# Kernel optimization log

Measured on AMD Instinct MI355X. Metric: run time of the kernel, lower is better.

The kernel has to match this reference:

```python
import jax, jax.numpy as jnp
import numpy as np

N_NODES = 100
F_IN = 65536
C_OUT = 60
ACTION_DIM = 100
N_EDGES = 2000


def setup_inputs() -> dict:
    key = jax.random.key(0)
    ks = jax.random.split(key, 16)
    s = 0.02
    return {
        "substrate_features": jax.random.normal(ks[0], (1, N_NODES, F_IN), jnp.float32),
        "edge_index": jax.random.randint(ks[1], (2, N_EDGES), 0, N_NODES, dtype=jnp.int32),
        "v_cpu_demand_t": jax.random.uniform(ks[2], (1,), jnp.float32),
        "v_bw_demand_t": jax.random.uniform(ks[3], (1,), jnp.float32),
        "num_pending_v_nodes_t": jax.random.uniform(ks[4], (1,), jnp.float32),
        "actor_w": jax.random.normal(ks[5], (3, F_IN, C_OUT), jnp.float32) * s,
        "actor_b": jax.random.normal(ks[6], (C_OUT,), jnp.float32) * s,
        "critic_w": jax.random.normal(ks[7], (3, F_IN, C_OUT), jnp.float32) * s,
        "critic_b": jax.random.normal(ks[8], (C_OUT,), jnp.float32) * s,
        "actor_fc_w": jax.random.normal(ks[9], (N_NODES * C_OUT + 3, ACTION_DIM), jnp.float32) * s,
        "actor_fc_b": jax.random.normal(ks[10], (ACTION_DIM,), jnp.float32) * s,
        "critic_fc_w": jax.random.normal(ks[11], (N_NODES * C_OUT + 3, 1), jnp.float32) * s,
        "critic_fc_b": jax.random.normal(ks[12], (1,), jnp.float32) * s,
    }


def cheb_conv(x, edge_index, W, b):
    # ChebConv, K=3, sym normalization, lambda_max=2 (PyG defaults).
    # With lambda_max=2 the scaled Laplacian is L_hat = -D^{-1/2} A D^{-1/2}
    # (diagonal becomes 0 after the -1 self-loop shift).
    # x: [1, N, F]; edge_index: [2, E]; W: [3, F, C]; b: [C]
    src, dst = edge_index[0], edge_index[1]
    n = x.shape[1]
    deg = jax.ops.segment_sum(jnp.ones(src.shape[0], x.dtype), src, num_segments=n)
    dis = jnp.where(deg > 0, jax.lax.rsqrt(jnp.where(deg > 0, deg, 1.0)), 0.0)
    norm = -(dis[src] * dis[dst])  # [E], L_hat off-diagonal entries
    x2 = x[0]  # [N, F]

    def prop(z):  # z: [N, F] -> L_hat @ z via gather/scatter over edges
        return jax.ops.segment_sum(z[src] * norm[:, None], dst, num_segments=n)

    Tx0 = x2
    Tx1 = prop(Tx0)
    Tx2 = 2.0 * prop(Tx1) - Tx0
    out = Tx0 @ W[0] + Tx1 @ W[1] + Tx2 @ W[2] + b  # [N, C]
    return out[None]  # [1, N, C]


def reference(substrate_features, edge_index, v_cpu_demand_t, v_bw_demand_t,
              num_pending_v_nodes_t, actor_w, actor_b, critic_w, critic_b,
              actor_fc_w, actor_fc_b, critic_fc_w, critic_fc_b):
    emb_a = jnp.tanh(cheb_conv(substrate_features, edge_index, actor_w, actor_b))
    emb_a = emb_a.reshape(1, -1)  # [1, N*60]
    emb_c = jnp.tanh(cheb_conv(substrate_features, edge_index, critic_w, critic_b))
    emb_c = emb_c.reshape(1, -1)
    extras = [v_cpu_demand_t[None], v_bw_demand_t[None], num_pending_v_nodes_t[None]]  # each [1,1]
    state_a = jnp.concatenate([emb_a] + extras, axis=1)  # [1, 6003]
    state_c = jnp.concatenate([emb_c] + extras, axis=1)
    logits = state_a @ actor_fc_w + actor_fc_b  # [1, action_dim]
    values = state_c @ critic_fc_w + critic_fc_b  # [1, 1]
    return (logits, values)
```

## Files before the change

kernel.cpp:

```cpp
#include <hip/hip_runtime.h>
#include <stdint.h>

#define F_IN 65536
#define NN 100
#define CO 60
#define G_SPLIT 128
#define KC (F_IN/G_SPLIT)
#define BK 64
#define NIT (KC/BK)

typedef short v8s __attribute__((ext_vector_type(8)));
typedef float v4f __attribute__((ext_vector_type(4)));

__device__ __forceinline__ unsigned int f2bf(float x){
  unsigned int u = __float_as_uint(x);
  u += 0x7fffu + ((u>>16)&1u);
  return u>>16;
}
__device__ __forceinline__ v4f mfma16(v8s a, v8s b, v4f c){
  return __builtin_amdgcn_mfma_f32_16x16x32_bf16(a,b,c,0,0,0);
}
__device__ __forceinline__ void cp16(const void* g, void* l){
  __builtin_amdgcn_global_load_lds((const __attribute__((address_space(1))) void*)g,
                                   (__attribute__((address_space(3))) void*)l, 16, 0, 0);
}

__global__ __launch_bounds__(256)
void k_cvt(const float* __restrict__ x, unsigned short* __restrict__ xb){
  int i = blockIdx.x*256 + threadIdx.x;
  float4 v = ((const float4*)x)[i];
  uint2 w;
  w.x = f2bf(v.x) | (f2bf(v.y)<<16);
  w.y = f2bf(v.z) | (f2bf(v.w)<<16);
  ((uint2*)xb)[i] = w;
}

__global__ __launch_bounds__(256,2)
void k_gemm(const unsigned short* __restrict__ xb, const float* __restrict__ aw,
            const float* __restrict__ cw, float* __restrict__ dst, int partial){
  const int s = blockIdx.x, g = blockIdx.y;
  const int k0 = s*KC;
  const int tid = threadIdx.x, wave = tid>>6, lane = tid&63, quad = lane>>4, nl = lane&15;
  const int c0 = wave*16, ccl = min(c0+nl, CO-1);

  __shared__ __align__(16) unsigned short Ab[2][112*64];
  __shared__ __align__(16) float          Wb[2][BK*CO];

  const float* W = (g<3) ? (aw + (size_t)g*F_IN*CO) : (cw + (size_t)(g-3)*F_IN*CO);

  const int nA = (wave<2) ? 4 : 3;
  const int nW = (wave<3) ? 4 : 3;
  const unsigned short* ag[4];
  unsigned int aoff[4];
  #pragma unroll
  for(int ti=0; ti<4; ++ti){
    int t   = wave + 4*ti;
    int row = 8*t + (lane>>3);
    int rcl = min(row, NN-1);
    int lch = (lane&7) ^ (row&7);
    ag[ti]  = xb + (size_t)rcl*F_IN + k0 + lch*8;
    aoff[ti] = t*512 + lane*8;
  }
  const float* wg[4];
  unsigned int woff[4];
  #pragma unroll
  for(int ti=0; ti<4; ++ti){
    int t = wave + 4*ti;
    wg[ti]   = W + (size_t)k0*CO + t*256 + lane*4;
    woff[ti] = t*256 + lane*4;
  }

  v4f acc[7];
  #pragma unroll
  for(int i=0;i<7;++i){ v4f z={0.f,0.f,0.f,0.f}; acc[i]=z; }

  #pragma unroll
  for(int ti=0; ti<4; ++ti) if(ti<nA) cp16(ag[ti], &Ab[0][aoff[ti]]);
  #pragma unroll
  for(int ti=0; ti<4; ++ti) if(ti<nW) cp16(wg[ti], &Wb[0][woff[ti]]);

  for(int it=0; it<NIT; ++it){
    __syncthreads();
    const int b = it&1;
    if(it+1 < NIT){
      const int nb = (it+1)&1;
      #pragma unroll
      for(int ti=0; ti<4; ++ti) if(ti<nA) cp16(ag[ti] + (it+1)*BK, &Ab[nb][aoff[ti]]);
      #pragma unroll
      for(int ti=0; ti<4; ++ti) if(ti<nW) cp16(wg[ti] + (size_t)(it+1)*BK*CO, &Wb[nb][woff[ti]]);
    }
    v8s fB0, fB1;
    #pragma unroll
    for(int j=0;j<8;++j){
      fB0[j] = (short)f2bf(Wb[b][(   quad*8+j)*CO + ccl]);
      fB1[j] = (short)f2bf(Wb[b][(32+quad*8+j)*CO + ccl]);
    }
    #pragma unroll
    for(int mt=0; mt<7; ++mt){
      int r  = mt*16 + nl;
      int p0 = ((quad ^ (r&7))*8);
      v8s a0 = *(const v8s*)&Ab[b][r*64 + p0];
      v8s a1 = *(const v8s*)&Ab[b][r*64 + (p0^32)];
      acc[mt] = mfma16(a0, fB0, acc[mt]);
      acc[mt] = mfma16(a1, fB1, acc[mt]);
    }
  }

  const int c = c0 + nl;
  if(c < CO){
    if(partial){
      float* pd = dst + ((size_t)g*G_SPLIT + s)*(NN*CO);
      #pragma unroll
      for(int mt=0;mt<7;++mt){
        #pragma unroll
        for(int i=0;i<4;++i){
          int m = mt*16 + quad*4 + i;
          if(m < NN) pd[m*CO + c] = acc[mt][i];
        }
      }
    } else {
      float* pd = dst + (size_t)g*(NN*CO);
      #pragma unroll
      for(int mt=0;mt<7;++mt){
        #pragma unroll
        for(int i=0;i<4;++i){
          int m = mt*16 + quad*4 + i;
          if(m < NN) atomicAdd(pd + m*CO + c, acc[mt][i]);
        }
      }
    }
  }
}

__global__ void k_reduce(const float* __restrict__ P, float* __restrict__ Y){
  int o = blockIdx.x*256 + threadIdx.x;
  if(o >= 6*NN*CO) return;
  int gg = o/(NN*CO), r = o - gg*(NN*CO);
  const float* p = P + (size_t)gg*G_SPLIT*(NN*CO) + (size_t)blockIdx.y*32*(NN*CO) + r;
  float a0=0.f,a1=0.f,a2=0.f,a3=0.f;
  #pragma unroll 2
  for(int s4=0;s4<32;s4+=4){
    a0 += p[(s4  )*(NN*CO)];
    a1 += p[(s4+1)*(NN*CO)];
    a2 += p[(s4+2)*(NN*CO)];
    a3 += p[(s4+3)*(NN*CO)];
  }
  atomicAdd(&Y[o], (a0+a1)+(a2+a3));
}

__global__ void k_cheb(const float* __restrict__ Y, const int* __restrict__ ei,
                       const float* __restrict__ ab, const float* __restrict__ cb,
                       float* __restrict__ emb){
  const int net = blockIdx.x / CO;
  const int c   = blockIdx.x % CO;
  const int t   = threadIdx.x;
  __shared__ float L[NN][NN+1];
  __shared__ float dis[NN];
  __shared__ int   deg[NN];
  __shared__ float y0[NN], y1[NN], y2[NN], zu[NN];

  for(int i=t;i<NN*(NN+1);i+=128) ((float*)L)[i]=0.f;
  if(t<NN) deg[t]=0;
  __syncthreads();
  for(int e=t;e<2000;e+=128) atomicAdd(&deg[ei[e]],1);
  __syncthreads();
  if(t<NN) dis[t] = deg[t]>0 ? rsqrtf((float)deg[t]) : 0.f;
  __syncthreads();
  for(int e=t;e<2000;e+=128){
    int s = ei[e], d = ei[2000+e];
    atomicAdd(&L[d][s], -dis[s]*dis[d]);
  }
  if(t<NN){
    const float* yb = Y + (size_t)net*3*NN*CO + t*CO + c;
    y0[t]=yb[0]; y1[t]=yb[NN*CO]; y2[t]=yb[2*NN*CO];
  }
  __syncthreads();
  if(t<NN){
    float s=0.f;
    #pragma unroll 4
    for(int j=0;j<NN;++j) s += L[t][j]*y2[j];
    zu[t] = y1[t] + 2.f*s;
  }
  __syncthreads();
  if(t<NN){
    float s=0.f;
    #pragma unroll 4
    for(int j=0;j<NN;++j) s += L[t][j]*zu[j];
    float b = (net==0) ? ab[c] : cb[c];
    emb[net*NN*CO + t*CO + c] = tanhf(y0[t] - y2[t] + s + b);
  }
}

#define FCB 25
__global__ void k_fc(const float* __restrict__ emb, const float* __restrict__ afw,
                     const float* __restrict__ afb, const float* __restrict__ cfw,
                     const float* __restrict__ cfb, const float* __restrict__ s0,
                     const float* __restrict__ s1, const float* __restrict__ s2,
                     float* __restrict__ out){
  const int b = blockIdx.x;
  const int t = threadIdx.x;
  if(b < FCB){
    const int jj = t & 127, half = t >> 7;
    if(jj < 100){
      const int i0 = b*240 + half*120;
      const float* w = afw + (size_t)i0*100 + jj;
      const float* e = emb + i0;
      float p = 0.f;
      #pragma unroll 4
      for(int i=0;i<120;++i) p += e[i]*w[(size_t)i*100];
      atomicAdd(&out[jj], p);
    }
  } else {
    float p = 0.f;
    const float* e = emb + 6000;
    for(int i=t;i<6000;i+=256) p += e[i]*cfw[i];
    #pragma unroll
    for(int o=32;o>0;o>>=1) p += __shfl_down(p,o,64);
    __shared__ float red[4];
    if((t&63)==0) red[t>>6]=p;
    __syncthreads();
    if(t==0){
      float tot = red[0]+red[1]+red[2]+red[3];
      out[100] = tot + s0[0]*cfw[6000] + s1[0]*cfw[6001] + s2[0]*cfw[6002] + cfb[0];
    }
    if(t<100){
      atomicAdd(&out[t], afb[t] + s0[0]*afw[600000+t] + s1[0]*afw[600100+t] + s2[0]*afw[600200+t]);
    }
  }
}

extern "C" void kernel_launch(void* const* d_in, const int* in_sizes, int n_in,
                              void* d_out, int out_size, void* d_ws, size_t ws_size,
                              hipStream_t stream){
  const float* x   = (const float*)d_in[0];
  const int*   ei  = (const int*)d_in[1];
  const float* s0  = (const float*)d_in[2];
  const float* s1  = (const float*)d_in[3];
  const float* s2  = (const float*)d_in[4];
  const float* aw  = (const float*)d_in[5];
  const float* ab  = (const float*)d_in[6];
  const float* cw  = (const float*)d_in[7];
  const float* cb  = (const float*)d_in[8];
  const float* afw = (const float*)d_in[9];
  const float* afb = (const float*)d_in[10];
  const float* cfw = (const float*)d_in[11];
  const float* cfb = (const float*)d_in[12];
  float* out = (float*)d_out;

  unsigned short* xb = (unsigned short*)d_ws;
  float* Y   = (float*)((char*)d_ws + 13107200);
  float* emb = Y + 6*NN*CO;
  float* P   = emb + 2*NN*CO;
  const size_t need_full = 13107200u + (size_t)(6*NN*CO + 2*NN*CO)*4 + (size_t)6*G_SPLIT*NN*CO*4;
  const int partial = (ws_size >= need_full) ? 1 : 0;

  hipMemsetAsync(Y, 0, 6*NN*CO*sizeof(float), stream);
  hipMemsetAsync(out, 0, 101*sizeof(float), stream);

  k_cvt<<<6400, 256, 0, stream>>>(x, xb);
  k_gemm<<<dim3(G_SPLIT,6), 256, 0, stream>>>(xb, aw, cw, partial ? P : Y, partial);
  if(partial){
    k_reduce<<<dim3((6*NN*CO+255)/256, 4), 256, 0, stream>>>(P, Y);
  }
  k_cheb<<<120, 128, 0, stream>>>(Y, ei, ab, cb, emb);
  k_fc<<<FCB+1, 256, 0, stream>>>(emb, afw, afb, cfw, cfb, s0, s1, s2, out);
}
```

Baseline: 216.3 us.

## Triple-buffer the GEMM K loop with smaller K tiles and explicit vmcnt waits

Replaces the double-buffered LDS pipeline in the split-K GEMM with a three-stage ring buffer, halving the K tile to 32 and issuing loads two iterations ahead. It uses explicit s_waitcnt vmcnt and raw s_barrier with scheduling barriers instead of __syncthreads, so compute on one stage can overlap two in-flight global-to-LDS copies. Load work is redistributed so each wave issues exactly four 16-byte copies per stage, with some duplicated copies to keep the pattern uniform. The smaller tile and launch bound of 3 aim to raise occupancy and hide memory latency. The cost is more loop iterations and barriers per block.

```diff
diff --git a/kernel.cpp b/kernel.cpp
--- a/kernel.cpp
+++ b/kernel.cpp
@@ -6,8 +6,12 @@
 #define CO 60
 #define G_SPLIT 128
 #define KC (F_IN/G_SPLIT)
-#define BK 64
+#define BK 32
 #define NIT (KC/BK)
+#define NBUF 3
+#define ABYTES (112*BK*2)
+#define WBYTES (BK*CO*4)
+#define BUFB (ABYTES+WBYTES)
 
 typedef short v8s __attribute__((ext_vector_type(8)));
 typedef float v4f __attribute__((ext_vector_type(4)));
@@ -35,7 +39,7 @@
   ((uint2*)xb)[i] = w;
 }
 
-__global__ __launch_bounds__(256,2)
+__global__ __launch_bounds__(256,3)
 void k_gemm(const unsigned short* __restrict__ xb, const float* __restrict__ aw,
             const float* __restrict__ cw, float* __restrict__ dst, int partial){
   const int s = blockIdx.x, g = blockIdx.y;
@@ -43,68 +47,63 @@
   const int tid = threadIdx.x, wave = tid>>6, lane = tid&63, quad = lane>>4, nl = lane&15;
   const int c0 = wave*16, ccl = min(c0+nl, CO-1);
 
-  __shared__ __align__(16) unsigned short Ab[2][112*64];
-  __shared__ __align__(16) float          Wb[2][BK*CO];
+  __shared__ __align__(16) char S[NBUF*BUFB];
 
   const float* W = (g<3) ? (aw + (size_t)g*F_IN*CO) : (cw + (size_t)(g-3)*F_IN*CO);
 
-  const int nA = (wave<2) ? 4 : 3;
-  const int nW = (wave<3) ? 4 : 3;
-  const unsigned short* ag[4];
-  unsigned int aoff[4];
+  const char* gsrc[4]; unsigned ldst[4]; unsigned gstep[4];
   #pragma unroll
-  for(int ti=0; ti<4; ++ti){
-    int t   = wave + 4*ti;
-    int row = 8*t + (lane>>3);
-    int rcl = min(row, NN-1);
-    int lch = (lane&7) ^ (row&7);
-    ag[ti]  = xb + (size_t)rcl*F_IN + k0 + lch*8;
-    aoff[ti] = t*512 + lane*8;
-  }
-  const float* wg[4];
-  unsigned int woff[4];
-  #pragma unroll
-  for(int ti=0; ti<4; ++ti){
-    int t = wave + 4*ti;
-    wg[ti]   = W + (size_t)k0*CO + t*256 + lane*4;
-    woff[ti] = t*256 + lane*4;
+  for(int i=0;i<4;++i){
+    int id = wave*4 + i;
+    if(id >= 15) id = 0;
+    if(id < 7){
+      int t = id;
+      int row = t*16 + (lane>>2);
+      int rcl = min(row, NN-1);
+      int lch = (lane&3) ^ (row&3);
+      gsrc[i]  = (const char*)(xb + (size_t)rcl*F_IN + k0) + lch*16;
+      gstep[i] = BK*2;
+      ldst[i]  = t*1024 + lane*16;
+    } else {
+      int t = id - 7;
+      int off = t*1024; if(off > WBYTES-1024) off = WBYTES-1024;
+      gsrc[i]  = (const char*)W + (size_t)k0*CO*4 + off + lane*16;
+      gstep[i] = WBYTES;
+      ldst[i]  = ABYTES + off + lane*16;
+    }
   }
 
   v4f acc[7];
   #pragma unroll
   for(int i=0;i<7;++i){ v4f z={0.f,0.f,0.f,0.f}; acc[i]=z; }
 
-  #pragma unroll
-  for(int ti=0; ti<4; ++ti) if(ti<nA) cp16(ag[ti], &Ab[0][aoff[ti]]);
-  #pragma unroll
-  for(int ti=0; ti<4; ++ti) if(ti<nW) cp16(wg[ti], &Wb[0][woff[ti]]);
-
-  for(int it=0; it<NIT; ++it){
-    __syncthreads();
-    const int b = it&1;
-    if(it+1 < NIT){
-      const int nb = (it+1)&1;
-      #pragma unroll
-      for(int ti=0; ti<4; ++ti) if(ti<nA) cp16(ag[ti] + (it+1)*BK, &Ab[nb][aoff[ti]]);
-      #pragma unroll
-      for(int ti=0; ti<4; ++ti) if(ti<nW) cp16(wg[ti] + (size_t)(it+1)*BK*CO, &Wb[nb][woff[ti]]);
-    }
-    v8s fB0, fB1;
-    #pragma unroll
-    for(int j=0;j<8;++j){
-      fB0[j] = (short)f2bf(Wb[b][(   quad*8+j)*CO + ccl]);
-      fB1[j] = (short)f2bf(Wb[b][(32+quad*8+j)*CO + ccl]);
-    }
-    #pragma unroll
-    for(int mt=0; mt<7; ++mt){
-      int r  = mt*16 + nl;
-      int p0 = ((quad ^ (r&7))*8);
-      v8s a0 = *(const v8s*)&Ab[b][r*64 + p0];
-      v8s a1 = *(const v8s*)&Ab[b][r*64 + (p0^32)];
-      acc[mt] = mfma16(a0, fB0, acc[mt]);
-      acc[mt] = mfma16(a1, fB1, acc[mt]);
-    }
-  }
+  #define ISSUE(it) { char* b_ = S + ((it)%NBUF)*BUFB; \
+    _Pragma("unroll") for(int i_=0;i_<4;++i_) cp16(gsrc[i_] + (size_t)(it)*gstep[i_], b_ + ldst[i_]); }
+
+  #define COMPUTE(it) { const char* b_ = S + ((it)%NBUF)*BUFB; \
+    const unsigned short* Ab_ = (const unsigned short*)b_; \
+    const float* Wb_ = (const float*)(b_ + ABYTES); \
+    v8s fB_; \
+    _Pragma("unroll") for(int j_=0;j_<8;++j_) fB_[j_] = (short)f2bf(Wb_[(quad*8+j_)*CO + ccl]); \
+    _Pragma("unroll") for(int mt_=0;mt_<7;++mt_){ \
+      int r_ = mt_*16 + nl; \
+      v8s a_ = *(const v8s*)(Ab_ + r_*BK + ((quad ^ (r_&3))*8)); \
+      acc[mt_] = mfma16(a_, fB_, acc[mt_]); } }
+
+  ISSUE(0); ISSUE(1);
+  for(int it=0; it<NIT-1; ++it){
+    __builtin_amdgcn_sched_barrier(0);
+    asm volatile("s_waitcnt vmcnt(4)" ::: "memory");
+    __builtin_amdgcn_s_barrier();
+    __builtin_amdgcn_sched_barrier(0);
+    if(it+2 < NIT) ISSUE(it+2);
+    COMPUTE(it);
+  }
+  __builtin_amdgcn_sched_barrier(0);
+  asm volatile("s_waitcnt vmcnt(0)" ::: "memory");
+  __builtin_amdgcn_s_barrier();
+  __builtin_amdgcn_sched_barrier(0);
+  COMPUTE(NIT-1);
 
   const int c = c0 + nl;
   if(c < CO){
```

After: 218.8 us. Within noise of the previous version (+1.2%).
